# Kernel optimization log

Measured on AMD Instinct MI355X. Metric: run time of the kernel, lower is better.

The kernel has to match this reference:

```python
import jax, jax.numpy as jnp
import numpy as np

K = 5   # reassembly kernel size
G = 1   # group size
S = 2   # upsample scale factor


def setup_inputs() -> dict:
    key = jax.random.key(0)
    kf, km = jax.random.split(key)
    N, C, H, W = 4, 256, 64, 64
    features = jax.random.normal(kf, (N, C, H, W), dtype=jnp.float32)
    # masks: [N, K*K*G, H*S, W*S]; CARAFE masks are non-negative (softmax-normalized upstream)
    masks = jax.random.uniform(km, (N, K * K * G, H * S, W * S), dtype=jnp.float32)
    return {"features": features, "masks": masks}


def _carafe(features, masks, k=K, g=G, s=S):
    # features: [N, C, H, W]; masks: [N, k*k*g, H*s, W*s]
    N, C, H, W = features.shape
    pad = (k - 1) // 2
    fp = jnp.pad(features, ((0, 0), (0, 0), (pad, pad), (pad, pad)))
    # unfold k x k neighborhoods at LOW resolution: [N, C, k*k, H, W]
    patches = jnp.stack(
        [fp[:, :, i:i + H, j:j + W] for i in range(k) for j in range(k)], axis=2
    )
    cg = C // g
    patches = patches.reshape(N, g, cg, k * k, H, W)
    # mask channel layout is [group, k*k]; split output pixels (i = h*s + p)
    m = masks.reshape(N, g, k * k, H, s, W, s)
    # out[n,g,c,h,p,w,q] = sum_k m[n,g,k,h,p,w,q] * patches[n,g,c,k,h,w]
    out = jnp.einsum('ngkhpwq,ngckhw->ngchpwq', m, patches)
    return out.reshape(N, C, H * s, W * s)


def reference(features, masks):
    return _carafe(features, masks)
```

## Files before the change

### kernel.cpp

```cpp
#include <hip/hip_runtime.h>


#define CN 4
#define CC 256
#define CH 64
#define CW 64
#define CK 5
#define OH 128
#define OW 128

typedef float f32x2 __attribute__((ext_vector_type(2)));

constexpr int TILE  = 16;
constexpr int SROWS = TILE + 4;
constexpr int LSTR  = 24;
constexpr int LBUF  = SROWS * LSTR;
constexpr int CPB   = 4;
constexpr int PPS   = CPB / 2;
constexpr int CH_PER_BLOCK = 32;
constexpr int NSTG  = CH_PER_BLOCK / CPB;

__global__ __launch_bounds__(256, 2)
void carafe_kernel(const float* __restrict__ feat,
                   const float* __restrict__ masks,
                   float* __restrict__ out)
{
    __shared__ float2 lds[2 * PPS * LBUF];

    const int tid  = threadIdx.x;
    const int wloc = tid & 15;
    const int hloc = tid >> 4;

    const int w0 = blockIdx.x * TILE;
    const int h0 = blockIdx.y * TILE;
    const int z  = blockIdx.z;
    const int n  = z >> 3;
    const int c0 = (z & 7) * CH_PER_BLOCK;

    const int r  = tid / 10;
    const int pc = tid % 10;
    const int q  = 2 * pc;
    const int gr = h0 - 2 + r;
    const int gc = w0 - 2 + q;
    const bool sv = (tid < 200) & (gr >= 0) & (gr < CH) & (gc >= 0) & (gc <= CW - 2);
    const int goff = sv ? (gr * CW + gc) : 0;
    const int l    = r * LSTR + q;

    const float* fbase = feat + (size_t)(n * CC + c0) * (CH * CW);

    const int oh0 = 2 * (h0 + hloc);
    const int ow0 = 2 * (w0 + wloc);
    const float* mp = masks + (((size_t)n * (CK * CK)) * OH + oh0) * OW + ow0;
    float2 m0[25], m1[25];
#pragma unroll
    for (int t = 0; t < 25; ++t) {
        m0[t] = *(const float2*)(mp + (size_t)t * (OH * OW));
        m1[t] = *(const float2*)(mp + (size_t)t * (OH * OW) + OW);
    }

    float2 pa[PPS], pb[PPS];

    auto loadStage = [&](int s) {
#pragma unroll
        for (int p = 0; p < PPS; ++p) {
            const float* f0 = fbase + (size_t)(s * CPB + 2 * p) * (CH * CW);
            pa[p] = sv ? *(const float2*)(f0 + goff) : make_float2(0.f, 0.f);
            pb[p] = sv ? *(const float2*)(f0 + CH * CW + goff) : make_float2(0.f, 0.f);
        }
    };
    auto writeStage = [&](int buf) {
        if (tid < 200) {
            float2* dst = &lds[buf * (PPS * LBUF)];
#pragma unroll
            for (int p = 0; p < PPS; ++p) {
                dst[p * LBUF + l]     = make_float2(pa[p].x, pb[p].x);
                dst[p * LBUF + l + 1] = make_float2(pa[p].y, pb[p].y);
            }
        }
    };

    loadStage(0);
    writeStage(0);
    loadStage(1);

    float* obase = out + (((size_t)(n * CC + c0) * OH + oh0) * OW + ow0);

    for (int s = 0; s < NSTG; ++s) {
        __syncthreads();

        if (s + 1 < NSTG) writeStage((s + 1) & 1);
        if (s + 2 < NSTG) loadStage(s + 2);

        const float2* sb = &lds[(s & 1) * (PPS * LBUF)];
#pragma unroll
        for (int p = 0; p < PPS; ++p) {
            const float2* lb = sb + p * LBUF + hloc * LSTR + wloc;
            float a00 = 0.f, a01 = 0.f, a10 = 0.f, a11 = 0.f;
            float b00 = 0.f, b01 = 0.f, b10 = 0.f, b11 = 0.f;
#pragma unroll
            for (int i = 0; i < CK; ++i) {
#pragma unroll
                for (int j = 0; j < CK; ++j) {
                    const int t = i * CK + j;
                    const float2 f = lb[i * LSTR + j];
                    a00 += m0[t].x * f.x; a01 += m0[t].y * f.x;
                    a10 += m1[t].x * f.x; a11 += m1[t].y * f.x;
                    b00 += m0[t].x * f.y; b01 += m0[t].y * f.y;
                    b10 += m1[t].x * f.y; b11 += m1[t].y * f.y;
                }
            }
            float* op0 = obase + (size_t)(s * CPB + 2 * p) * (OH * OW);
            float* op1 = op0 + (OH * OW);
            __builtin_nontemporal_store((f32x2){a00, a01}, (f32x2*)op0);
            __builtin_nontemporal_store((f32x2){a10, a11}, (f32x2*)(op0 + OW));
            __builtin_nontemporal_store((f32x2){b00, b01}, (f32x2*)op1);
            __builtin_nontemporal_store((f32x2){b10, b11}, (f32x2*)(op1 + OW));
        }
    }
}

extern "C" void kernel_launch(void* const* d_in, const int* in_sizes, int n_in,
                              void* d_out, int out_size, void* d_ws, size_t ws_size,
                              hipStream_t stream) {
    const float* feat  = (const float*)d_in[0];
    const float* masks = (const float*)d_in[1];
    float* out = (float*)d_out;

    dim3 grid(CW / TILE, CH / TILE, CN * (CC / CH_PER_BLOCK));
    dim3 block(256);
    hipLaunchKernelGGL(carafe_kernel, grid, block, 0, stream, feat, masks, out);
}
```

Measured before the change: 105.5 us.

## Shrink per-block channel count and stream masks per tap for higher occupancy

Each block now handles 8 channels in a single pass instead of 32 channels through a double-buffered pipeline. Mask values are streamed one tap at a time with a one-tap prefetch rather than held as 50 float2 registers. Launch bounds rise to 4 blocks per CU. This lowers register pressure and raises parallelism, at the cost of re-reading masks 4x more often and dropping the cross-stage overlap of loads with compute.

Result: faster. 102.9 us (-2.4%).

```diff
diff --git a/kernel.cpp b/kernel.cpp
--- a/kernel.cpp
+++ b/kernel.cpp
@@ -15,17 +15,15 @@
 constexpr int SROWS = TILE + 4;
 constexpr int LSTR  = 24;
 constexpr int LBUF  = SROWS * LSTR;
-constexpr int CPB   = 4;
+constexpr int CPB   = 8;
 constexpr int PPS   = CPB / 2;
-constexpr int CH_PER_BLOCK = 32;
-constexpr int NSTG  = CH_PER_BLOCK / CPB;
 
-__global__ __launch_bounds__(256, 2)
+__global__ __launch_bounds__(256, 4)
 void carafe_kernel(const float* __restrict__ feat,
                    const float* __restrict__ masks,
                    float* __restrict__ out)
 {
-    __shared__ float2 lds[2 * PPS * LBUF];
+    __shared__ float2 lds[PPS * LBUF];
 
     const int tid  = threadIdx.x;
     const int wloc = tid & 15;
@@ -34,12 +32,11 @@
     const int w0 = blockIdx.x * TILE;
     const int h0 = blockIdx.y * TILE;
     const int z  = blockIdx.z;
-    const int n  = z >> 3;
-    const int c0 = (z & 7) * CH_PER_BLOCK;
+    const int n  = z >> 5;
+    const int c0 = (z & 31) * CPB;
 
     const int r  = tid / 10;
-    const int pc = tid % 10;
-    const int q  = 2 * pc;
+    const int q  = 2 * (tid % 10);
     const int gr = h0 - 2 + r;
     const int gc = w0 - 2 + q;
     const bool sv = (tid < 200) & (gr >= 0) & (gr < CH) & (gc >= 0) & (gc <= CW - 2);
@@ -48,74 +45,70 @@
 
     const float* fbase = feat + (size_t)(n * CC + c0) * (CH * CW);
 
+    float2 pa[PPS], pb[PPS];
+#pragma unroll
+    for (int p = 0; p < PPS; ++p) {
+        const float* f0 = fbase + (size_t)(2 * p) * (CH * CW);
+        pa[p] = sv ? *(const float2*)(f0 + goff) : make_float2(0.f, 0.f);
+        pb[p] = sv ? *(const float2*)(f0 + CH * CW + goff) : make_float2(0.f, 0.f);
+    }
+    if (tid < 200) {
+#pragma unroll
+        for (int p = 0; p < PPS; ++p) {
+            lds[p * LBUF + l]     = make_float2(pa[p].x, pb[p].x);
+            lds[p * LBUF + l + 1] = make_float2(pa[p].y, pb[p].y);
+        }
+    }
+
     const int oh0 = 2 * (h0 + hloc);
     const int ow0 = 2 * (w0 + wloc);
     const float* mp = masks + (((size_t)n * (CK * CK)) * OH + oh0) * OW + ow0;
-    float2 m0[25], m1[25];
+
+    float2 cm0 = *(const float2*)(mp);
+    float2 cm1 = *(const float2*)(mp + OW);
+
+    __syncthreads();
+
+    float2 a0[CPB], a1[CPB];
 #pragma unroll
-    for (int t = 0; t < 25; ++t) {
-        m0[t] = *(const float2*)(mp + (size_t)t * (OH * OW));
-        m1[t] = *(const float2*)(mp + (size_t)t * (OH * OW) + OW);
+    for (int c = 0; c < CPB; ++c) {
+        a0[c] = make_float2(0.f, 0.f);
+        a1[c] = make_float2(0.f, 0.f);
     }
 
-    float2 pa[PPS], pb[PPS];
+    const float2* lb = &lds[hloc * LSTR + wloc];
 
-    auto loadStage = [&](int s) {
+#pragma unroll
+    for (int t = 0; t < CK * CK; ++t) {
+        const int i = t / CK, j = t % CK;
+
+        float2 nm0 = cm0, nm1 = cm1;
+        if (t + 1 < CK * CK) {
+            nm0 = *(const float2*)(mp + (size_t)(t + 1) * (OH * OW));
+            nm1 = *(const float2*)(mp + (size_t)(t + 1) * (OH * OW) + OW);
+        }
+
+        float2 f[PPS];
+#pragma unroll
+        for (int p = 0; p < PPS; ++p)
+            f[p] = lb[p * LBUF + i * LSTR + j];
+
 #pragma unroll
         for (int p = 0; p < PPS; ++p) {
-            const float* f0 = fbase + (size_t)(s * CPB + 2 * p) * (CH * CW);
-            pa[p] = sv ? *(const float2*)(f0 + goff) : make_float2(0.f, 0.f);
-            pb[p] = sv ? *(const float2*)(f0 + CH * CW + goff) : make_float2(0.f, 0.f);
+            a0[2 * p].x     += cm0.x * f[p].x;  a0[2 * p].y     += cm0.y * f[p].x;
+            a1[2 * p].x     += cm1.x * f[p].x;  a1[2 * p].y     += cm1.y * f[p].x;
+            a0[2 * p + 1].x += cm0.x * f[p].y;  a0[2 * p + 1].y += cm0.y * f[p].y;
+            a1[2 * p + 1].x += cm1.x * f[p].y;  a1[2 * p + 1].y += cm1.y * f[p].y;
         }
-    };
-    auto writeStage = [&](int buf) {
-        if (tid < 200) {
-            float2* dst = &lds[buf * (PPS * LBUF)];
-#pragma unroll
-            for (int p = 0; p < PPS; ++p) {
-                dst[p * LBUF + l]     = make_float2(pa[p].x, pb[p].x);
-                dst[p * LBUF + l + 1] = make_float2(pa[p].y, pb[p].y);
-            }
-        }
-    };
-
-    loadStage(0);
-    writeStage(0);
-    loadStage(1);
+        cm0 = nm0; cm1 = nm1;
+    }
 
     float* obase = out + (((size_t)(n * CC + c0) * OH + oh0) * OW + ow0);
-
-    for (int s = 0; s < NSTG; ++s) {
-        __syncthreads();
-
-        if (s + 1 < NSTG) writeStage((s + 1) & 1);
-        if (s + 2 < NSTG) loadStage(s + 2);
-
-        const float2* sb = &lds[(s & 1) * (PPS * LBUF)];
 #pragma unroll
-        for (int p = 0; p < PPS; ++p) {
-            const float2* lb = sb + p * LBUF + hloc * LSTR + wloc;
-            float a00 = 0.f, a01 = 0.f, a10 = 0.f, a11 = 0.f;
-            float b00 = 0.f, b01 = 0.f, b10 = 0.f, b11 = 0.f;
-#pragma unroll
-            for (int i = 0; i < CK; ++i) {
-#pragma unroll
-                for (int j = 0; j < CK; ++j) {
-                    const int t = i * CK + j;
-                    const float2 f = lb[i * LSTR + j];
-                    a00 += m0[t].x * f.x; a01 += m0[t].y * f.x;
-                    a10 += m1[t].x * f.x; a11 += m1[t].y * f.x;
-                    b00 += m0[t].x * f.y; b01 += m0[t].y * f.y;
-                    b10 += m1[t].x * f.y; b11 += m1[t].y * f.y;
-                }
-            }
-            float* op0 = obase + (size_t)(s * CPB + 2 * p) * (OH * OW);
-            float* op1 = op0 + (OH * OW);
-            __builtin_nontemporal_store((f32x2){a00, a01}, (f32x2*)op0);
-            __builtin_nontemporal_store((f32x2){a10, a11}, (f32x2*)(op0 + OW));
-            __builtin_nontemporal_store((f32x2){b00, b01}, (f32x2*)op1);
-            __builtin_nontemporal_store((f32x2){b10, b11}, (f32x2*)(op1 + OW));
-        }
+    for (int c = 0; c < CPB; ++c) {
+        float* op = obase + (size_t)c * (OH * OW);
+        __builtin_nontemporal_store((f32x2){a0[c].x, a0[c].y}, (f32x2*)op);
+        __builtin_nontemporal_store((f32x2){a1[c].x, a1[c].y}, (f32x2*)(op + OW));
     }
 }
 
@@ -126,7 +119,7 @@
     const float* masks = (const float*)d_in[1];
     float* out = (float*)d_out;
 
-    dim3 grid(CW / TILE, CH / TILE, CN * (CC / CH_PER_BLOCK));
+    dim3 grid(CW / TILE, CH / TILE, CN * (CC / CPB));
     dim3 block(256);
     hipLaunchKernelGGL(carafe_kernel, grid, block, 0, stream, feat, masks, out);
 }
```
